# Kernel optimization log

Measured on AMD Instinct MI355X. Metric: run time of the kernel, lower is better.

The kernel has to match this reference:

```python
import jax, jax.numpy as jnp
import numpy as np

NUM_HEADS = 8
IN_DIM = 384
HEAD_DIM = IN_DIM // NUM_HEADS  # 48


def setup_inputs() -> dict:
    key = jax.random.key(0)
    ks = jax.random.split(key, 6)
    B, N, M, C = 4, 4096, 1024, 384
    q_x = jax.random.normal(ks[0], (B, N, C), dtype=jnp.float32)
    kv_x = jax.random.normal(ks[1], (B, M, C), dtype=jnp.float32)
    s = C ** -0.5  # fan-in style init scale
    Wq = jax.random.normal(ks[2], (C, IN_DIM), dtype=jnp.float32) * s
    Wkv = jax.random.normal(ks[3], (C, 2 * IN_DIM), dtype=jnp.float32) * s
    Wproj = jax.random.normal(ks[4], (IN_DIM, IN_DIM), dtype=jnp.float32) * (IN_DIM ** -0.5)
    bproj = jnp.zeros((IN_DIM,), dtype=jnp.float32)
    return {"q_x": q_x, "kv_x": kv_x, "Wq": Wq, "Wkv": Wkv, "Wproj": Wproj, "bproj": bproj}


def reference(q_x, kv_x, Wq, Wkv, Wproj, bproj):
    B, N, C = q_x.shape
    M = kv_x.shape[1]
    scale = HEAD_DIM ** -0.5
    # q: [B, H, N, hd]
    q = (q_x @ Wq).reshape(B, N, NUM_HEADS, HEAD_DIM).transpose(0, 2, 1, 3)
    # k, v: [B, H, M, hd]
    kv = (kv_x @ Wkv).reshape(B, M, 2, NUM_HEADS, HEAD_DIM).transpose(2, 0, 3, 1, 4)
    k, v = kv[0], kv[1]
    # attention scores [B, H, N, M]
    attn = jax.nn.softmax(jnp.einsum('bhnd,bhmd->bhnm', q, k) * scale, axis=-1)
    x = jnp.einsum('bhnm,bhmd->bhnd', attn, v)  # [B, H, N, hd]
    x = x.transpose(0, 2, 1, 3).reshape(B, N, IN_DIM)
    x = x @ Wproj + bproj
    # sr_ratio == 1 residual: add raw q projection back
    q_res = q.transpose(0, 2, 1, 3).reshape(B, N, IN_DIM)
    return q_res + x
```

## Files before the change

### kernel.cpp

```cpp
#include <hip/hip_runtime.h>
#include <hip/hip_bf16.h>
#include <math.h>

#define B_ 4
#define N_ 4096
#define M_ 1024
#define C_ 384
#define NH_ 8
#define HD_ 48

typedef float f32x4 __attribute__((ext_vector_type(4)));
typedef short bf16x8 __attribute__((ext_vector_type(8)));

typedef __attribute__((address_space(3))) unsigned int lds_uint;
typedef const __attribute__((address_space(1))) unsigned int glob_uint;

__device__ __forceinline__ void gld_lds16(const void* g, void* l) {
    __builtin_amdgcn_global_load_lds((glob_uint*)g, (lds_uint*)l, 16, 0, 0);
}

__device__ __forceinline__ unsigned short f2bf(float x) {
    unsigned int u = __builtin_bit_cast(unsigned int, x);
    return (unsigned short)((u + 0x7FFFu + ((u >> 16) & 1u)) >> 16);
}
__device__ __forceinline__ unsigned short f2bf_trunc(float x) {
    return (unsigned short)(__builtin_bit_cast(unsigned int, x) >> 16);
}
__device__ __forceinline__ float bf2f(unsigned short x) {
    return __builtin_bit_cast(float, (unsigned int)x << 16);
}
__device__ __forceinline__ float fast_exp2(float x) {
#if __has_builtin(__builtin_amdgcn_exp2f)
    return __builtin_amdgcn_exp2f(x);
#else
    return exp2f(x);
#endif
}
__device__ __forceinline__ uint2 pack4_rne(float a, float b, float c, float d) {
    uint2 r;
    r.x = (unsigned int)f2bf(a) | ((unsigned int)f2bf(b) << 16);
    r.y = (unsigned int)f2bf(c) | ((unsigned int)f2bf(d) << 16);
    return r;
}

#define QSCALE 0.20823490983597203f

__global__ __launch_bounds__(256)
void conv_act(const float* __restrict__ a, unsigned short* __restrict__ da,
              const float* __restrict__ b, unsigned short* __restrict__ db)
{
    size_t i4 = (size_t)blockIdx.x * 256 + threadIdx.x;
    const float* src; unsigned short* dst;
    if (i4 < 1572864u) { src = a; dst = da; }
    else { src = b; dst = db; i4 -= 1572864u; }
    float4 v = *(const float4*)&src[i4 * 4];
    *(uint2*)&dst[i4 * 4] = pack4_rne(v.x, v.y, v.z, v.w);
}

__global__ __launch_bounds__(256)
void transpose_w3(const float* __restrict__ Wq, const float* __restrict__ Wkv,
                  const float* __restrict__ Wproj,
                  unsigned short* __restrict__ Wq_t, unsigned short* __restrict__ Wkv_t,
                  unsigned short* __restrict__ Wproj_t)
{
    __shared__ unsigned short T[64 * 72];
    const int tid = threadIdx.x;
    int bid = blockIdx.x;
    const float* W; unsigned short* Wt; int N, kt, nt;
    if (bid < 36)       { W = Wq;    Wt = Wq_t;    N = 384; kt = bid / 6;  nt = bid - kt * 6; }
    else if (bid < 108) { bid -= 36;  W = Wkv;   Wt = Wkv_t;   N = 768; kt = bid / 12; nt = bid - kt * 12; }
    else                { bid -= 108; W = Wproj; Wt = Wproj_t; N = 384; kt = bid / 6;  nt = bid - kt * 6; }
    const int k0 = kt * 64, n0 = nt * 64;

    #pragma unroll
    for (int it = 0; it < 4; ++it) {
        int k = it * 16 + (tid >> 4);
        int n4 = (tid & 15) * 4;
        float4 v = *(const float4*)&W[(size_t)(k0 + k) * N + n0 + n4];
        T[(n4 + 0) * 72 + k] = f2bf(v.x);
        T[(n4 + 1) * 72 + k] = f2bf(v.y);
        T[(n4 + 2) * 72 + k] = f2bf(v.z);
        T[(n4 + 3) * 72 + k] = f2bf(v.w);
    }
    __syncthreads();
    #pragma unroll
    for (int i = 0; i < 2; ++i) {
        int s = tid + 256 * i;
        int n = s >> 3, part = s & 7;
        *(uint4*)&Wt[(size_t)(n0 + n) * C_ + k0 + part * 8] = *(const uint4*)&T[n * 72 + part * 8];
    }
}

__device__ __forceinline__ void stage128(const unsigned short* src, unsigned short* lds,
                                         int kk, int tid) {
    #pragma unroll
    for (int r = 0; r < 4; ++r) {
        int off = r * 256 + tid;
        int row = off >> 3;
        int c = off & 7;
        int gc = c ^ (row & 7);
        gld_lds16(src + (size_t)row * C_ + kk + gc * 8, lds + (size_t)off * 8);
    }
}
__device__ __forceinline__ bf16x8 frag_ld(const unsigned short* lds, int row, int chunk) {
    return *(const bf16x8*)&lds[row * 64 + ((chunk ^ (row & 7)) << 3)];
}

#define GEMM_CORE(Aptr, Wptr)                                                        \
    f32x4 acc[4][4];                                                                 \
    _Pragma("unroll")                                                                \
    for (int rt = 0; rt < 4; ++rt)                                                   \
        _Pragma("unroll")                                                            \
        for (int ct = 0; ct < 4; ++ct) acc[rt][ct] = (f32x4){0.f, 0.f, 0.f, 0.f};    \
    const int wrow0 = (wave & 1) * 64;                                               \
    const int wcol0 = (wave >> 1) * 64;                                              \
    for (int kk = 0; kk < C_; kk += 64) {                                            \
        __syncthreads();                                                             \
        stage128(Aptr, As, kk, tid);                                                 \
        stage128(Wptr, Ws, kk, tid);                                                 \
        __syncthreads();                                                             \
        _Pragma("unroll")                                                            \
        for (int ks = 0; ks < 2; ++ks) {                                             \
            bf16x8 af[4], wf[4];                                                     \
            _Pragma("unroll")                                                        \
            for (int rt = 0; rt < 4; ++rt)                                           \
                af[rt] = frag_ld(As, wrow0 + rt * 16 + ln, ks * 4 + quad);           \
            _Pragma("unroll")                                                        \
            for (int ct = 0; ct < 4; ++ct)                                           \
                wf[ct] = frag_ld(Ws, wcol0 + ct * 16 + ln, ks * 4 + quad);           \
            _Pragma("unroll")                                                        \
            for (int rt = 0; rt < 4; ++rt)                                           \
                _Pragma("unroll")                                                    \
                for (int ct = 0; ct < 4; ++ct)                                       \
                    acc[rt][ct] = __builtin_amdgcn_mfma_f32_16x16x32_bf16(           \
                        wf[ct], af[rt], acc[rt][ct], 0, 0, 0);                       \
        }                                                                            \
    }

__global__ __launch_bounds__(256)
void gemm_qkv(const unsigned short* __restrict__ qx, const unsigned short* __restrict__ kvx,
              const unsigned short* __restrict__ Wqt, const unsigned short* __restrict__ Wkvt,
              unsigned short* __restrict__ qbf, unsigned short* __restrict__ qres,
              unsigned short* __restrict__ kbf, unsigned short* __restrict__ vbf)
{
    __shared__ unsigned short As[128 * 64];
    __shared__ unsigned short Ws[128 * 64];
    const int tid = threadIdx.x;
    const int wave = tid >> 6;
    const int lane = tid & 63;
    const int ln = lane & 15;
    const int quad = lane >> 4;

    int bid = blockIdx.x;
    int mode, row0, col0;
    const unsigned short *A, *Wt;
    if (bid < 384) { mode = 0; A = qx;  Wt = Wqt;  row0 = (bid / 3) * 128; col0 = (bid % 3) * 128; }
    else { bid -= 384; mode = 1; A = kvx; Wt = Wkvt; row0 = (bid / 6) * 128; col0 = (bid % 6) * 128; }

    GEMM_CORE(A + (size_t)row0 * C_, Wt + (size_t)col0 * C_)

    #pragma unroll
    for (int rt = 0; rt < 4; ++rt) {
        int grow = row0 + wrow0 + rt * 16 + ln;
        #pragma unroll
        for (int ct = 0; ct < 4; ++ct) {
            int col = col0 + wcol0 + ct * 16 + quad * 4;
            f32x4 v = acc[rt][ct];
            if (mode == 0) {
                *(uint2*)&qres[(size_t)grow * C_ + col] = pack4_rne(v[0], v[1], v[2], v[3]);
                int b = grow >> 12, n = grow & (N_ - 1);
                int h = col / HD_, d = col - h * HD_;
                *(uint2*)&qbf[(((size_t)(b * NH_ + h) * N_) + n) * HD_ + d] =
                    pack4_rne(v[0] * QSCALE, v[1] * QSCALE, v[2] * QSCALE, v[3] * QSCALE);
            } else {
                int b = grow >> 10, m = grow & (M_ - 1);
                if (col < C_) {
                    int h = col / HD_, d = col - h * HD_;
                    *(uint2*)&kbf[(((size_t)(b * NH_ + h) * M_) + m) * HD_ + d] =
                        pack4_rne(v[0], v[1], v[2], v[3]);
                } else {
                    int c2 = col - C_;
                    int h = c2 / HD_, d = c2 - h * HD_;
                    size_t base = ((size_t)(b * NH_ + h) * HD_ + d) * M_ + m;
                    #pragma unroll
                    for (int r = 0; r < 4; ++r) vbf[base + (size_t)r * M_] = f2bf(v[r]);
                }
            }
        }
    }
}

__global__ __launch_bounds__(256)
void gemm_out(const unsigned short* __restrict__ A, const unsigned short* __restrict__ Wt,
              float* __restrict__ out0,
              const unsigned short* __restrict__ addend, const float* __restrict__ bias)
{
    __shared__ unsigned short As[128 * 64];
    __shared__ unsigned short Ws[128 * 64];
    const int tid = threadIdx.x;
    const int wave = tid >> 6;
    const int lane = tid & 63;
    const int ln = lane & 15;
    const int quad = lane >> 4;
    const int row0 = (blockIdx.x / 3) * 128;
    const int col0 = (blockIdx.x % 3) * 128;

    GEMM_CORE(A + (size_t)row0 * C_, Wt + (size_t)col0 * C_)

    #pragma unroll
    for (int rt = 0; rt < 4; ++rt) {
        int grow = row0 + wrow0 + rt * 16 + ln;
        #pragma unroll
        for (int ct = 0; ct < 4; ++ct) {
            int col = col0 + wcol0 + ct * 16 + quad * 4;
            f32x4 v = acc[rt][ct];
            size_t idx = (size_t)grow * C_ + col;
            uint2 ad = *(const uint2*)&addend[idx];
            float4 bi = *(const float4*)&bias[col];
            float4 o;
            o.x = v[0] + bf2f((unsigned short)(ad.x & 0xFFFF)) + bi.x;
            o.y = v[1] + bf2f((unsigned short)(ad.x >> 16))    + bi.y;
            o.z = v[2] + bf2f((unsigned short)(ad.y & 0xFFFF)) + bi.z;
            o.w = v[3] + bf2f((unsigned short)(ad.y >> 16))    + bi.w;
            *(float4*)&out0[idx] = o;
        }
    }
}

__global__ __launch_bounds__(256, 2)
void attn_mfma(const unsigned short* __restrict__ qbf,
               const unsigned short* __restrict__ kbf,
               const unsigned short* __restrict__ vbf,
               unsigned short* __restrict__ of)
{
    __shared__ unsigned short P[4][64 * 72];

    const int tid = threadIdx.x;
    const int wave = tid >> 6;
    const int lane = tid & 63;
    const int ln = lane & 15;
    const int quad = lane >> 4;
    const int bh = blockIdx.x;
    const int n0w = blockIdx.y * 256 + wave * 64;

    const bf16x8 zero8 = (bf16x8){0, 0, 0, 0, 0, 0, 0, 0};

    bf16x8 qb[4][2];
    #pragma unroll
    for (int qt = 0; qt < 4; ++qt) {
        const unsigned short* qp = qbf + ((size_t)bh * N_ + n0w + qt * 16 + ln) * HD_;
        qb[qt][0] = *(const bf16x8*)(qp + quad * 8);
        qb[qt][1] = *(const bf16x8*)(qp + 32 + quad * 8);
        if (quad >= 2) qb[qt][1] = zero8;
    }

    f32x4 O[3][4];
    #pragma unroll
    for (int ot = 0; ot < 3; ++ot)
        #pragma unroll
        for (int qt = 0; qt < 4; ++qt) O[ot][qt] = (f32x4){0.f, 0.f, 0.f, 0.f};
    float rs[4] = {0.f, 0.f, 0.f, 0.f};

    const unsigned short* kb = kbf + (size_t)bh * M_ * HD_;
    const unsigned short* vb = vbf + (size_t)bh * HD_ * M_;
    unsigned short* Pw = &P[wave][0];

    for (int mt = 0; mt < M_ / 64; ++mt) {
        bf16x8 va[3][2];
        #pragma unroll
        for (int ot = 0; ot < 3; ++ot) {
            const unsigned short* vp = vb + (size_t)(ot * 16 + ln) * M_ + mt * 64;
            va[ot][0] = *(const bf16x8*)(vp + quad * 8);
            va[ot][1] = *(const bf16x8*)(vp + 32 + quad * 8);
        }
        bf16x8 ka[4][2];
        #pragma unroll
        for (int t = 0; t < 4; ++t) {
            const unsigned short* kp = kb + (size_t)(mt * 64 + t * 16 + ln) * HD_;
            ka[t][0] = *(const bf16x8*)(kp + quad * 8);
            ka[t][1] = *(const bf16x8*)(kp + 32 + quad * 8);
            if (quad >= 2) ka[t][1] = zero8;
        }

        #pragma unroll
        for (int t = 0; t < 4; ++t) {
            #pragma unroll
            for (int qt = 0; qt < 4; ++qt) {
                f32x4 s = (f32x4){0.f, 0.f, 0.f, 0.f};
                s = __builtin_amdgcn_mfma_f32_16x16x32_bf16(ka[t][0], qb[qt][0], s, 0, 0, 0);
                s = __builtin_amdgcn_mfma_f32_16x16x32_bf16(ka[t][1], qb[qt][1], s, 0, 0, 0);
                float p0 = fast_exp2(s[0]);
                float p1 = fast_exp2(s[1]);
                float p2 = fast_exp2(s[2]);
                float p3 = fast_exp2(s[3]);
                rs[qt] += (p0 + p1) + (p2 + p3);
                uint2 pk;
                pk.x = (unsigned int)f2bf_trunc(p0) | ((unsigned int)f2bf_trunc(p1) << 16);
                pk.y = (unsigned int)f2bf_trunc(p2) | ((unsigned int)f2bf_trunc(p3) << 16);
                *(uint2*)&Pw[(qt * 16 + ln) * 72 + t * 16 + quad * 4] = pk;
            }
        }

        #pragma unroll
        for (int qt = 0; qt < 4; ++qt) {
            const unsigned short* Pr = &Pw[(qt * 16 + ln) * 72];
            bf16x8 pb0 = *(const bf16x8*)(Pr + quad * 8);
            bf16x8 pb1 = *(const bf16x8*)(Pr + 32 + quad * 8);
            #pragma unroll
            for (int ot = 0; ot < 3; ++ot) {
                O[ot][qt] = __builtin_amdgcn_mfma_f32_16x16x32_bf16(va[ot][0], pb0, O[ot][qt], 0, 0, 0);
                O[ot][qt] = __builtin_amdgcn_mfma_f32_16x16x32_bf16(va[ot][1], pb1, O[ot][qt], 0, 0, 0);
            }
        }
    }

    float inv[4];
    #pragma unroll
    for (int qt = 0; qt < 4; ++qt) {
        float x = rs[qt];
        x += __shfl_xor(x, 16);
        x += __shfl_xor(x, 32);
        inv[qt] = 1.0f / x;
    }

    const int b = bh >> 3, h = bh & 7;
    #pragma unroll
    for (int ot = 0; ot < 3; ++ot)
        #pragma unroll
        for (int qt = 0; qt < 4; ++qt) {
            size_t grow = (size_t)b * N_ + n0w + qt * 16 + ln;
            int gcol = h * HD_ + ot * 16 + quad * 4;
            *(uint2*)&of[grow * C_ + gcol] =
                pack4_rne(O[ot][qt][0] * inv[qt], O[ot][qt][1] * inv[qt],
                          O[ot][qt][2] * inv[qt], O[ot][qt][3] * inv[qt]);
        }
}

extern "C" void kernel_launch(void* const* d_in, const int* in_sizes, int n_in,
                              void* d_out, int out_size, void* d_ws, size_t ws_size,
                              hipStream_t stream) {
    const float* q_x   = (const float*)d_in[0];
    const float* kv_x  = (const float*)d_in[1];
    const float* Wq    = (const float*)d_in[2];
    const float* Wkv   = (const float*)d_in[3];
    const float* Wproj = (const float*)d_in[4];
    const float* bproj = (const float*)d_in[5];
    float* out = (float*)d_out;

    unsigned short* qbf     = (unsigned short*)d_ws;
    unsigned short* kbf     = qbf     + 6291456;
    unsigned short* vbf     = kbf     + 1572864;
    unsigned short* qres    = vbf     + 1572864;
    unsigned short* of      = qres    + 6291456;
    unsigned short* qx_bf   = of      + 6291456;
    unsigned short* kvx_bf  = qx_bf   + 6291456;
    unsigned short* Wq_t    = kvx_bf  + 1572864;
    unsigned short* Wkv_t   = Wq_t    + 147456;
    unsigned short* Wproj_t = Wkv_t   + 294912;

    dim3 blk(256);

    conv_act<<<dim3(7680), blk, 0, stream>>>(q_x, qx_bf, kv_x, kvx_bf);
    transpose_w3<<<dim3(144), blk, 0, stream>>>(Wq, Wkv, Wproj, Wq_t, Wkv_t, Wproj_t);

    gemm_qkv<<<dim3(576), blk, 0, stream>>>(
        qx_bf, kvx_bf, Wq_t, Wkv_t, qbf, qres, kbf, vbf);

    attn_mfma<<<dim3(32, 16), blk, 0, stream>>>(qbf, kbf, vbf, of);

    gemm_out<<<dim3(384), blk, 0, stream>>>(of, Wproj_t, out, qres, bproj);
}
```

Baseline: 171.3 us.

## Split attention KV range across two wave groups and merge prep kernels

The attention block grows to 512 threads. Each group of four waves handles half of the KV tiles for the same query rows, and the partial outputs and row sums are then combined through shared memory. This doubles the waves per query tile, which should improve latency hiding and occupancy. The activation conversion and weight transpose kernels are also merged into one launch to cut launch overhead. In exchange it adds a shared-memory reduction with two block barriers and doubles the LDS used per block.

```diff
diff --git a/kernel.cpp b/kernel.cpp
--- a/kernel.cpp
+++ b/kernel.cpp
@@ -46,26 +46,28 @@
 #define QSCALE 0.20823490983597203f
 
 __global__ __launch_bounds__(256)
-void conv_act(const float* __restrict__ a, unsigned short* __restrict__ da,
-              const float* __restrict__ b, unsigned short* __restrict__ db)
-{
-    size_t i4 = (size_t)blockIdx.x * 256 + threadIdx.x;
-    const float* src; unsigned short* dst;
-    if (i4 < 1572864u) { src = a; dst = da; }
-    else { src = b; dst = db; i4 -= 1572864u; }
-    float4 v = *(const float4*)&src[i4 * 4];
-    *(uint2*)&dst[i4 * 4] = pack4_rne(v.x, v.y, v.z, v.w);
-}
-
-__global__ __launch_bounds__(256)
-void transpose_w3(const float* __restrict__ Wq, const float* __restrict__ Wkv,
-                  const float* __restrict__ Wproj,
-                  unsigned short* __restrict__ Wq_t, unsigned short* __restrict__ Wkv_t,
-                  unsigned short* __restrict__ Wproj_t)
+void prep(const float* __restrict__ qx_f, unsigned short* __restrict__ qx_bf,
+          const float* __restrict__ kvx_f, unsigned short* __restrict__ kvx_bf,
+          const float* __restrict__ Wq, const float* __restrict__ Wkv,
+          const float* __restrict__ Wproj,
+          unsigned short* __restrict__ Wq_t, unsigned short* __restrict__ Wkv_t,
+          unsigned short* __restrict__ Wproj_t)
 {
     __shared__ unsigned short T[64 * 72];
     const int tid = threadIdx.x;
     int bid = blockIdx.x;
+
+    if (bid < 7680) {
+        size_t i4 = (size_t)bid * 256 + tid;
+        const float* src; unsigned short* dst;
+        if (i4 < 1572864u) { src = qx_f; dst = qx_bf; }
+        else { src = kvx_f; dst = kvx_bf; i4 -= 1572864u; }
+        float4 v = *(const float4*)&src[i4 * 4];
+        *(uint2*)&dst[i4 * 4] = pack4_rne(v.x, v.y, v.z, v.w);
+        return;
+    }
+
+    bid -= 7680;
     const float* W; unsigned short* Wt; int N, kt, nt;
     if (bid < 36)       { W = Wq;    Wt = Wq_t;    N = 384; kt = bid / 6;  nt = bid - kt * 6; }
     else if (bid < 108) { bid -= 36;  W = Wkv;   Wt = Wkv_t;   N = 768; kt = bid / 12; nt = bid - kt * 12; }
@@ -227,21 +229,23 @@
     }
 }
 
-__global__ __launch_bounds__(256, 2)
+__global__ __launch_bounds__(512, 4)
 void attn_mfma(const unsigned short* __restrict__ qbf,
                const unsigned short* __restrict__ kbf,
                const unsigned short* __restrict__ vbf,
                unsigned short* __restrict__ of)
 {
-    __shared__ unsigned short P[4][64 * 72];
+    __shared__ unsigned short P[8][64 * 72];
 
     const int tid = threadIdx.x;
     const int wave = tid >> 6;
+    const int qwave = wave & 3;
+    const int mhalf = wave >> 2;
     const int lane = tid & 63;
     const int ln = lane & 15;
     const int quad = lane >> 4;
     const int bh = blockIdx.x;
-    const int n0w = blockIdx.y * 256 + wave * 64;
+    const int n0w = blockIdx.y * 256 + qwave * 64;
 
     const bf16x8 zero8 = (bf16x8){0, 0, 0, 0, 0, 0, 0, 0};
 
@@ -265,7 +269,8 @@
     const unsigned short* vb = vbf + (size_t)bh * HD_ * M_;
     unsigned short* Pw = &P[wave][0];
 
-    for (int mt = 0; mt < M_ / 64; ++mt) {
+    const int mt0 = mhalf * 8;
+    for (int mt = mt0; mt < mt0 + 8; ++mt) {
         bf16x8 va[3][2];
         #pragma unroll
         for (int ot = 0; ot < 3; ++ot) {
@@ -314,6 +319,34 @@
         }
     }
 
+    __syncthreads();
+    float* exb = (float*)&P[0][0];
+    if (mhalf) {
+        float* ex = exb + ((size_t)qwave * 64 + lane) * 52;
+        #pragma unroll
+        for (int ot = 0; ot < 3; ++ot)
+            #pragma unroll
+            for (int qt = 0; qt < 4; ++qt)
+                *(f32x4*)&ex[(ot * 4 + qt) * 4] = O[ot][qt];
+        #pragma unroll
+        for (int qt = 0; qt < 4; ++qt) ex[48 + qt] = rs[qt];
+    }
+    __syncthreads();
+    if (mhalf) return;
+
+    {
+        const float* ex = exb + ((size_t)qwave * 64 + lane) * 52;
+        #pragma unroll
+        for (int ot = 0; ot < 3; ++ot)
+            #pragma unroll
+            for (int qt = 0; qt < 4; ++qt) {
+                f32x4 u = *(const f32x4*)&ex[(ot * 4 + qt) * 4];
+                O[ot][qt] += u;
+            }
+        #pragma unroll
+        for (int qt = 0; qt < 4; ++qt) rs[qt] += ex[48 + qt];
+    }
+
     float inv[4];
     #pragma unroll
     for (int qt = 0; qt < 4; ++qt) {
@@ -360,13 +393,13 @@
 
     dim3 blk(256);
 
-    conv_act<<<dim3(7680), blk, 0, stream>>>(q_x, qx_bf, kv_x, kvx_bf);
-    transpose_w3<<<dim3(144), blk, 0, stream>>>(Wq, Wkv, Wproj, Wq_t, Wkv_t, Wproj_t);
+    prep<<<dim3(7824), blk, 0, stream>>>(q_x, qx_bf, kv_x, kvx_bf,
+                                         Wq, Wkv, Wproj, Wq_t, Wkv_t, Wproj_t);
 
     gemm_qkv<<<dim3(576), blk, 0, stream>>>(
         qx_bf, kvx_bf, Wq_t, Wkv_t, qbf, qres, kbf, vbf);
 
-    attn_mfma<<<dim3(32, 16), blk, 0, stream>>>(qbf, kbf, vbf, of);
+    attn_mfma<<<dim3(32, 16), dim3(512), 0, stream>>>(qbf, kbf, vbf, of);
 
     gemm_out<<<dim3(384), blk, 0, stream>>>(of, Wproj_t, out, qres, bproj);
 }
```

Result: slower. 330.0 us (+92.6%).

## Stage K/V tiles through double-buffered LDS and merge prep kernels

Applied to the files above, without the earlier changes.

The attention kernel now has the whole block cooperatively load each 64-row K and V tile into swizzled, double-buffered shared memory with async global-to-LDS loads. The next tile is prefetched while the current one is computed. Previously each of the four waves read K/V fragments from global memory on its own. The activation-conversion and weight-transpose kernels are also merged into one launch to save a kernel launch. The added LDS (32KB) may reduce occupancy, and the per-tile barrier adds synchronisation cost.

```diff
diff --git a/kernel.cpp b/kernel.cpp
--- a/kernel.cpp
+++ b/kernel.cpp
@@ -46,26 +46,28 @@
 #define QSCALE 0.20823490983597203f
 
 __global__ __launch_bounds__(256)
-void conv_act(const float* __restrict__ a, unsigned short* __restrict__ da,
-              const float* __restrict__ b, unsigned short* __restrict__ db)
-{
-    size_t i4 = (size_t)blockIdx.x * 256 + threadIdx.x;
-    const float* src; unsigned short* dst;
-    if (i4 < 1572864u) { src = a; dst = da; }
-    else { src = b; dst = db; i4 -= 1572864u; }
-    float4 v = *(const float4*)&src[i4 * 4];
-    *(uint2*)&dst[i4 * 4] = pack4_rne(v.x, v.y, v.z, v.w);
-}
-
-__global__ __launch_bounds__(256)
-void transpose_w3(const float* __restrict__ Wq, const float* __restrict__ Wkv,
-                  const float* __restrict__ Wproj,
-                  unsigned short* __restrict__ Wq_t, unsigned short* __restrict__ Wkv_t,
-                  unsigned short* __restrict__ Wproj_t)
+void prep(const float* __restrict__ qx_f, unsigned short* __restrict__ qx_bf,
+          const float* __restrict__ kvx_f, unsigned short* __restrict__ kvx_bf,
+          const float* __restrict__ Wq, const float* __restrict__ Wkv,
+          const float* __restrict__ Wproj,
+          unsigned short* __restrict__ Wq_t, unsigned short* __restrict__ Wkv_t,
+          unsigned short* __restrict__ Wproj_t)
 {
     __shared__ unsigned short T[64 * 72];
     const int tid = threadIdx.x;
     int bid = blockIdx.x;
+
+    if (bid < 7680) {
+        size_t i4 = (size_t)bid * 256 + tid;
+        const float* src; unsigned short* dst;
+        if (i4 < 1572864u) { src = qx_f; dst = qx_bf; }
+        else { src = kvx_f; dst = kvx_bf; i4 -= 1572864u; }
+        float4 v = *(const float4*)&src[i4 * 4];
+        *(uint2*)&dst[i4 * 4] = pack4_rne(v.x, v.y, v.z, v.w);
+        return;
+    }
+
+    bid -= 7680;
     const float* W; unsigned short* Wt; int N, kt, nt;
     if (bid < 36)       { W = Wq;    Wt = Wq_t;    N = 384; kt = bid / 6;  nt = bid - kt * 6; }
     else if (bid < 108) { bid -= 36;  W = Wkv;   Wt = Wkv_t;   N = 768; kt = bid / 12; nt = bid - kt * 12; }
@@ -233,6 +235,8 @@
                const unsigned short* __restrict__ vbf,
                unsigned short* __restrict__ of)
 {
+    __shared__ unsigned short Ks[2][64 * 64];
+    __shared__ unsigned short Vs[2][64 * 64];
     __shared__ unsigned short P[4][64 * 72];
 
     const int tid = threadIdx.x;
@@ -245,6 +249,10 @@
 
     const bf16x8 zero8 = (bf16x8){0, 0, 0, 0, 0, 0, 0, 0};
 
+    const unsigned short* kb = kbf + (size_t)bh * M_ * HD_;
+    const unsigned short* vb = vbf + (size_t)bh * HD_ * M_;
+    unsigned short* Pw = &P[wave][0];
+
     bf16x8 qb[4][2];
     #pragma unroll
     for (int qt = 0; qt < 4; ++qt) {
@@ -261,25 +269,47 @@
         for (int qt = 0; qt < 4; ++qt) O[ot][qt] = (f32x4){0.f, 0.f, 0.f, 0.f};
     float rs[4] = {0.f, 0.f, 0.f, 0.f};
 
-    const unsigned short* kb = kbf + (size_t)bh * M_ * HD_;
-    const unsigned short* vb = vbf + (size_t)bh * HD_ * M_;
-    unsigned short* Pw = &P[wave][0];
-
-    for (int mt = 0; mt < M_ / 64; ++mt) {
+#define STAGE_KV(buf, mt)                                                     \
+    {                                                                         \
+        const int m0s = (mt) * 64;                                            \
+        _Pragma("unroll")                                                     \
+        for (int r = 0; r < 2; ++r) {                                         \
+            int s = r * 256 + tid;                                            \
+            int row = s >> 3, gc = (s & 7) ^ (row & 7);                       \
+            gld_lds16(kb + (size_t)(m0s + row) * HD_ + gc * 8,                \
+                      &Ks[buf][(size_t)s * 8]);                               \
+        }                                                                     \
+        _Pragma("unroll")                                                     \
+        for (int r = 0; r < 2; ++r) {                                         \
+            int s = r * 256 + tid;                                            \
+            int row = s >> 3, gc = (s & 7) ^ (row & 7);                       \
+            gld_lds16(vb + (size_t)row * M_ + m0s + gc * 8,                   \
+                      &Vs[buf][(size_t)s * 8]);                               \
+        }                                                                     \
+    }
+
+    STAGE_KV(0, 0)
+    asm volatile("s_waitcnt vmcnt(0)" ::: "memory");
+    __builtin_amdgcn_s_barrier();
+
+    for (int mt = 0; mt < 16; ++mt) {
+        const int cur = mt & 1;
+        if (mt < 15) STAGE_KV(cur ^ 1, mt + 1)
+
+        const unsigned short* KsC = &Ks[cur][0];
+        const unsigned short* VsC = &Vs[cur][0];
+
         bf16x8 va[3][2];
         #pragma unroll
         for (int ot = 0; ot < 3; ++ot) {
-            const unsigned short* vp = vb + (size_t)(ot * 16 + ln) * M_ + mt * 64;
-            va[ot][0] = *(const bf16x8*)(vp + quad * 8);
-            va[ot][1] = *(const bf16x8*)(vp + 32 + quad * 8);
+            va[ot][0] = frag_ld(VsC, ot * 16 + ln, quad);
+            va[ot][1] = frag_ld(VsC, ot * 16 + ln, 4 + quad);
         }
         bf16x8 ka[4][2];
         #pragma unroll
         for (int t = 0; t < 4; ++t) {
-            const unsigned short* kp = kb + (size_t)(mt * 64 + t * 16 + ln) * HD_;
-            ka[t][0] = *(const bf16x8*)(kp + quad * 8);
-            ka[t][1] = *(const bf16x8*)(kp + 32 + quad * 8);
-            if (quad >= 2) ka[t][1] = zero8;
+            ka[t][0] = frag_ld(KsC, t * 16 + ln, quad);
+            ka[t][1] = (quad < 2) ? frag_ld(KsC, t * 16 + ln, 4 + quad) : zero8;
         }
 
         #pragma unroll
@@ -312,7 +342,13 @@
                 O[ot][qt] = __builtin_amdgcn_mfma_f32_16x16x32_bf16(va[ot][1], pb1, O[ot][qt], 0, 0, 0);
             }
         }
-    }
+
+        asm volatile("s_waitcnt vmcnt(0)" ::: "memory");
+        __builtin_amdgcn_sched_barrier(0);
+        __builtin_amdgcn_s_barrier();
+        __builtin_amdgcn_sched_barrier(0);
+    }
+#undef STAGE_KV
 
     float inv[4];
     #pragma unroll
@@ -360,8 +396,8 @@
 
     dim3 blk(256);
 
-    conv_act<<<dim3(7680), blk, 0, stream>>>(q_x, qx_bf, kv_x, kvx_bf);
-    transpose_w3<<<dim3(144), blk, 0, stream>>>(Wq, Wkv, Wproj, Wq_t, Wkv_t, Wproj_t);
+    prep<<<dim3(7824), blk, 0, stream>>>(q_x, qx_bf, kv_x, kvx_bf,
+                                         Wq, Wkv, Wproj, Wq_t, Wkv_t, Wproj_t);
 
     gemm_qkv<<<dim3(576), blk, 0, stream>>>(
         qx_bf, kvx_bf, Wq_t, Wkv_t, qbf, qres, kbf, vbf);
```

Result: no change. 169.7 us (-0.9%).
